# Performance work log

Measured on AMD Instinct MI355X. Metric: run time of the kernel, lower is better.

## Reference

```python
import jax, jax.numpy as jnp
import numpy as np

D_IN = 2048
D_SAE = 16384
N_RANGES = 4
CTX = 128  # batch == context_length
CHUNK = D_SAE // N_RANGES
LN_EPS = 1e-5


def setup_inputs() -> dict:
    key = jax.random.key(0)
    k1, k2, k3, k4 = jax.random.split(key, 4)
    acts = jax.random.normal(k1, (CTX, D_IN), dtype=jnp.float32)
    # orthogonal-init stand-ins: unit-variance columns
    W_enc_ranges = jax.random.normal(k2, (N_RANGES, D_IN, CHUNK), dtype=jnp.float32) / np.sqrt(D_IN)
    W_dec = jax.random.normal(k3, (D_SAE, D_IN), dtype=jnp.float32) / np.sqrt(D_SAE)
    pos_embeddings = jax.random.normal(k4, (N_RANGES, D_IN), dtype=jnp.float32) * 0.02
    return {
        "acts": acts,
        "W_enc_ranges": W_enc_ranges,
        "b_enc": jnp.zeros((D_SAE,), jnp.float32),
        "b_dec": jnp.zeros((D_IN,), jnp.float32),
        "pos_embeddings": pos_embeddings,
        "ln_weight": jnp.ones((D_SAE,), jnp.float32),
        "ln_bias": jnp.zeros((D_SAE,), jnp.float32),
        "W_dec": W_dec,
    }


def reference(acts, W_enc_ranges, b_enc, b_dec, pos_embeddings, ln_weight, ln_bias, W_dec):
    B, d_in = acts.shape
    n_ranges, _, chunk = W_enc_ranges.shape
    range_size = B // n_ranges  # positions are contiguous blocks per range
    d_sae = n_ranges * chunk

    # gather per position range: [n_ranges, range_size, d_in]
    x = acts.reshape(n_ranges, range_size, d_in)
    x = x + pos_embeddings[:, None, :] - b_dec  # (input + pos_emb) - b_dec

    # per-range GEMM + bias
    pre = jnp.einsum("rbd,rds->rbs", x, W_enc_ranges) + b_enc.reshape(n_ranges, 1, chunk)

    # per-range LayerNorm over the chunk (sliced gamma/beta), biased variance
    mu = jnp.mean(pre, axis=-1, keepdims=True)
    var = jnp.mean(jnp.square(pre - mu), axis=-1, keepdims=True)
    normed = (pre - mu) * jax.lax.rsqrt(var + LN_EPS)
    normed = normed * ln_weight.reshape(n_ranges, 1, chunk) + ln_bias.reshape(n_ranges, 1, chunk)
    feat = jax.nn.relu(normed)  # [n_ranges, range_size, chunk]

    # scatter into block-diagonal encoded [B, d_sae]
    encoded = jnp.zeros((B, d_sae), acts.dtype)
    for r in range(n_ranges):
        encoded = encoded.at[r * range_size:(r + 1) * range_size,
                             r * chunk:(r + 1) * chunk].set(feat[r])

    # decode
    decoded = encoded @ W_dec + b_dec
    return decoded
```

## Files before the change

### kernel.cpp

```cpp
#include <hip/hip_runtime.h>
#include <hip/hip_bf16.h>
#include <stdint.h>


#define D_IN   2048
#define CHUNK  4096
#define RS     32
#define LN_EPS 1e-5f

typedef __attribute__((ext_vector_type(8))) short bf16x8;
typedef __attribute__((ext_vector_type(4))) float f32x4;

#define AS1 __attribute__((address_space(1)))
#define AS3 __attribute__((address_space(3)))

__device__ __forceinline__ void gload_lds16(const float* g, float* l) {
  __builtin_amdgcn_global_load_lds((const AS1 unsigned int*)g,
                                   (AS3 unsigned int*)l, 16, 0, 0);
}

__device__ __forceinline__ unsigned short f2bf(float f) {
  unsigned int u = __float_as_uint(f);
  u += 0x7fffu + ((u >> 16) & 1u);
  return (unsigned short)(u >> 16);
}

__global__ __launch_bounds__(256) void prep_kernel(
    const float* __restrict__ acts, const float* __restrict__ pos,
    const float* __restrict__ bdec, unsigned short* __restrict__ xfrag) {
  unsigned tid = blockIdx.x * 256u + threadIdx.x;
  unsigned lane = tid & 63u, kt = (tid >> 6) & 63u, mt = (tid >> 12) & 1u, r = tid >> 13;
  unsigned m  = mt * 16 + (lane & 15u);
  unsigned k0 = kt * 32 + (lane >> 4) * 8;
  const float* ap = acts + (size_t)(r * RS + m) * D_IN + k0;
  const float* pp = pos  + (size_t)r * D_IN + k0;
  const float* bp = bdec + k0;
  bf16x8 v;
#pragma unroll
  for (int j = 0; j < 8; ++j) v[j] = (short)f2bf(ap[j] + pp[j] - bp[j]);
  *reinterpret_cast<bf16x8*>(xfrag + (size_t)tid * 8) = v;
}

__global__ __launch_bounds__(256) void enc_kernel(
    const unsigned short* __restrict__ xfrag, const float* __restrict__ Wenc,
    float* __restrict__ pre_part) {
  const unsigned r = blockIdx.x >> 8, h = (blockIdx.x >> 7) & 1u, nt = blockIdx.x & 127u;
  const unsigned n0 = nt * 32;
  const unsigned w = threadIdx.x >> 6, lane = threadIdx.x & 63u;
  const unsigned mt = w >> 1, nsub = w & 1u;
  const unsigned col = lane & 15u, g = lane >> 4;

  __shared__ float tiles[2][64 * 32];

  const unsigned srow = lane >> 3;
  const unsigned scol = (lane & 7u) * 4u;
  const float* gbase = Wenc + ((size_t)(r * D_IN + h * 1024)) * CHUNK + n0 + scol;
  const unsigned short* xa = xfrag + ((size_t)(r * 2 + mt) * 64) * 512 + (size_t)lane * 8;

  f32x4 acc = {0.f, 0.f, 0.f, 0.f};

  auto stageW = [&](unsigned s, unsigned b) {
#pragma unroll
    for (int l = 0; l < 2; ++l) {
      const float* gp = gbase + (size_t)(s * 64 + w * 16 + l * 8 + srow) * CHUNK;
      gload_lds16(gp, &tiles[b][(w * 2 + l) * 256]);
    }
  };

  stageW(0, 0);
  __syncthreads();

  unsigned cur = 0;
  for (unsigned s = 0; s < 16; ++s) {
    if (s + 1 < 16) stageW(s + 1, cur ^ 1);
#pragma unroll
    for (int t = 0; t < 2; ++t) {
      unsigned kt = h * 32 + s * 2 + t;
      bf16x8 a = *(const bf16x8*)(xa + (size_t)kt * 512);
      const float* tb = &tiles[cur][(t * 32 + g * 8) * 32 + nsub * 16 + col];
      bf16x8 bfrag;
#pragma unroll
      for (int j = 0; j < 8; ++j) bfrag[j] = (short)f2bf(tb[j * 32]);
      acc = __builtin_amdgcn_mfma_f32_16x16x32_bf16(a, bfrag, acc, 0, 0, 0);
    }
    __syncthreads();
    cur ^= 1;
  }

  float* pp = pre_part + (size_t)h * 128 * CHUNK;
  const unsigned nc = n0 + nsub * 16 + col;
#pragma unroll
  for (int i = 0; i < 4; ++i) {
    unsigned row = r * RS + mt * 16 + g * 4 + i;
    pp[(size_t)row * CHUNK + nc] = acc[i];
  }
}

__global__ __launch_bounds__(256) void lnpack_kernel(
    const float* __restrict__ pre_part, const float* __restrict__ benc,
    const float* __restrict__ gamma, const float* __restrict__ beta,
    unsigned short* __restrict__ featfrag) {
  const unsigned row = blockIdx.x;
  const unsigned r = row >> 5, m = row & 31u;
  const unsigned t = threadIdx.x;
  const unsigned c0 = t * 16;

  const float* p0 = pre_part + (size_t)row * CHUNK + c0;
  const float* p1 = p0 + (size_t)128 * CHUNK;
  const float* bb = benc + (size_t)r * CHUNK + c0;

  float v[16];
  float s = 0.f, q = 0.f;
#pragma unroll
  for (int j = 0; j < 16; ++j) {
    v[j] = p0[j] + p1[j] + bb[j];
    s += v[j]; q += v[j] * v[j];
  }
#pragma unroll
  for (int off = 1; off < 64; off <<= 1) {
    s += __shfl_xor(s, off, 64);
    q += __shfl_xor(q, off, 64);
  }
  __shared__ float ls[4], lq[4];
  if ((t & 63u) == 0) { ls[t >> 6] = s; lq[t >> 6] = q; }
  __syncthreads();
  s = ls[0] + ls[1] + ls[2] + ls[3];
  q = lq[0] + lq[1] + lq[2] + lq[3];
  float mu  = s * (1.f / CHUNK);
  float var = q * (1.f / CHUNK) - mu * mu;
  float rsd = rsqrtf(var + LN_EPS);

  const float* gp = gamma + (size_t)r * CHUNK + c0;
  const float* bp = beta  + (size_t)r * CHUNK + c0;
  const unsigned mt = m >> 4;
#pragma unroll
  for (int half = 0; half < 2; ++half) {
    bf16x8 o;
#pragma unroll
    for (int j = 0; j < 8; ++j) {
      float x = (v[half * 8 + j] - mu) * rsd * gp[half * 8 + j] + bp[half * 8 + j];
      o[j] = (short)f2bf(fmaxf(x, 0.f));
    }
    unsigned k = c0 + half * 8;
    unsigned kt = k >> 5, grp = (k >> 3) & 3u, ln = (m & 15u) + 16u * grp;
    *(bf16x8*)(featfrag + (((size_t)(r * 2 + mt) * 128 + kt) * 64 + ln) * 8) = o;
  }
}

__global__ __launch_bounds__(256) void dec_kernel(
    const unsigned short* __restrict__ featfrag, const float* __restrict__ Wdec,
    float* __restrict__ part) {
  const unsigned r = blockIdx.x >> 8, h = (blockIdx.x >> 6) & 3u, nt = blockIdx.x & 63u;
  const unsigned n0 = nt * 32;
  const unsigned w = threadIdx.x >> 6, lane = threadIdx.x & 63u;
  const unsigned mt = w >> 1, nsub = w & 1u;
  const unsigned col = lane & 15u, g = lane >> 4;

  __shared__ float tiles[2][64 * 32];

  const unsigned srow = lane >> 3;
  const unsigned scol = (lane & 7u) * 4u;
  const float* gbase = Wdec + ((size_t)(r * CHUNK + h * 1024)) * D_IN + n0 + scol;
  const unsigned short* fa = featfrag + ((size_t)(r * 2 + mt) * 128) * 512 + (size_t)lane * 8;

  f32x4 acc = {0.f, 0.f, 0.f, 0.f};

  auto stageW = [&](unsigned s, unsigned b) {
#pragma unroll
    for (int l = 0; l < 2; ++l) {
      const float* gp = gbase + (size_t)(s * 64 + w * 16 + l * 8 + srow) * D_IN;
      gload_lds16(gp, &tiles[b][(w * 2 + l) * 256]);
    }
  };

  stageW(0, 0);
  __syncthreads();

  unsigned cur = 0;
  for (unsigned s = 0; s < 16; ++s) {
    if (s + 1 < 16) stageW(s + 1, cur ^ 1);
#pragma unroll
    for (int t = 0; t < 2; ++t) {
      unsigned kt = h * 32 + s * 2 + t;
      bf16x8 a = *(const bf16x8*)(fa + (size_t)kt * 512);
      const float* tb = &tiles[cur][(t * 32 + g * 8) * 32 + nsub * 16 + col];
      bf16x8 bfrag;
#pragma unroll
      for (int j = 0; j < 8; ++j) bfrag[j] = (short)f2bf(tb[j * 32]);
      acc = __builtin_amdgcn_mfma_f32_16x16x32_bf16(a, bfrag, acc, 0, 0, 0);
    }
    __syncthreads();
    cur ^= 1;
  }

  float* pp = part + (size_t)h * 128 * D_IN;
  const unsigned nc = n0 + nsub * 16 + col;
#pragma unroll
  for (int i = 0; i < 4; ++i) {
    unsigned row = r * RS + mt * 16 + g * 4 + i;
    pp[(size_t)row * D_IN + nc] = acc[i];
  }
}

__global__ __launch_bounds__(256) void finish_kernel(
    const float* __restrict__ part, const float* __restrict__ bdec,
    float* __restrict__ out) {
  unsigned i = blockIdx.x * 256u + threadIdx.x;
  const size_t stride = (size_t)128 * D_IN / 4;
  f32x4 a0 = ((const f32x4*)part)[i];
  f32x4 a1 = ((const f32x4*)part)[i + stride];
  f32x4 a2 = ((const f32x4*)part)[i + 2 * stride];
  f32x4 a3 = ((const f32x4*)part)[i + 3 * stride];
  f32x4 c  = ((const f32x4*)bdec)[i & 511u];
  f32x4 o;
#pragma unroll
  for (int j = 0; j < 4; ++j) o[j] = a0[j] + a1[j] + a2[j] + a3[j] + c[j];
  ((f32x4*)out)[i] = o;
}

extern "C" void kernel_launch(void* const* d_in, const int* in_sizes, int n_in,
                              void* d_out, int out_size, void* d_ws, size_t ws_size,
                              hipStream_t stream) {
  const float* acts = (const float*)d_in[0];
  const float* Wenc = (const float*)d_in[1];
  const float* benc = (const float*)d_in[2];
  const float* bdec = (const float*)d_in[3];
  const float* pos  = (const float*)d_in[4];
  const float* lnw  = (const float*)d_in[5];
  const float* lnb  = (const float*)d_in[6];
  const float* Wdec = (const float*)d_in[7];
  float* out = (float*)d_out;

  char* ws = (char*)d_ws;
  unsigned short* xfrag   = (unsigned short*)ws;
  float* pre_part         = (float*)(ws + 512 * 1024);
  unsigned short* featfrg = (unsigned short*)(ws + 512 * 1024 + 4 * 1024 * 1024);
  float* part             = (float*)(ws + 512 * 1024 + 5 * 1024 * 1024);

  prep_kernel  <<<128,  256, 0, stream>>>(acts, pos, bdec, xfrag);
  enc_kernel   <<<1024, 256, 0, stream>>>(xfrag, Wenc, pre_part);
  lnpack_kernel<<<128,  256, 0, stream>>>(pre_part, benc, lnw, lnb, featfrg);
  dec_kernel   <<<1024, 256, 0, stream>>>(featfrg, Wdec, part);
  finish_kernel<<<256,  256, 0, stream>>>(part, bdec, out);
}
```

Before: 71.49 us.

## Split K across waves with private LDS tiles and reduce partials at end

Each wave in the encoder and decoder GEMM blocks now owns a private double-buffered LDS tile and a separate K-slice. It computes all four 16x16 output subtiles, reusing each converted B fragment across both M tiles. Per-iteration __syncthreads are replaced by per-wave vmcnt waits, and a single LDS reduction across waves runs at the end. This is meant to halve redundant fp32->bf16 conversions of W and remove block-wide barriers from the main loop. The cost is more accumulator registers, a final reduction pass, and reliance on hand-written waitcnt counts being correct.

```diff
diff --git a/kernel.cpp b/kernel.cpp
--- a/kernel.cpp
+++ b/kernel.cpp
@@ -24,6 +24,8 @@
   u += 0x7fffu + ((u >> 16) & 1u);
   return (unsigned short)(u >> 16);
 }
+
+#define MFMA16 __builtin_amdgcn_mfma_f32_16x16x32_bf16
 
 __global__ __launch_bounds__(256) void prep_kernel(
     const float* __restrict__ acts, const float* __restrict__ pos,
@@ -47,52 +49,92 @@
   const unsigned r = blockIdx.x >> 8, h = (blockIdx.x >> 7) & 1u, nt = blockIdx.x & 127u;
   const unsigned n0 = nt * 32;
   const unsigned w = threadIdx.x >> 6, lane = threadIdx.x & 63u;
-  const unsigned mt = w >> 1, nsub = w & 1u;
   const unsigned col = lane & 15u, g = lane >> 4;
 
-  __shared__ float tiles[2][64 * 32];
-
-  const unsigned srow = lane >> 3;
-  const unsigned scol = (lane & 7u) * 4u;
-  const float* gbase = Wenc + ((size_t)(r * D_IN + h * 1024)) * CHUNK + n0 + scol;
-  const unsigned short* xa = xfrag + ((size_t)(r * 2 + mt) * 64) * 512 + (size_t)lane * 8;
-
-  f32x4 acc = {0.f, 0.f, 0.f, 0.f};
+  __shared__ float smem[8192];
+  float* mytile = smem + w * 2048;
+
+  const unsigned srow = lane >> 3, scol = (lane & 7u) * 4u;
+  const float* gbase = Wenc
+      + ((size_t)(r * D_IN + h * 1024 + w * 32 + srow)) * CHUNK + n0 + scol;
+  const unsigned short* xa0 = xfrag + ((size_t)(r * 2 + 0) * 64) * 512 + (size_t)lane * 8;
+  const unsigned short* xa1 = xfrag + ((size_t)(r * 2 + 1) * 64) * 512 + (size_t)lane * 8;
+
+  f32x4 acc00 = {0.f,0.f,0.f,0.f}, acc01 = acc00, acc10 = acc00, acc11 = acc00;
 
   auto stageW = [&](unsigned s, unsigned b) {
 #pragma unroll
-    for (int l = 0; l < 2; ++l) {
-      const float* gp = gbase + (size_t)(s * 64 + w * 16 + l * 8 + srow) * CHUNK;
-      gload_lds16(gp, &tiles[b][(w * 2 + l) * 256]);
+    for (int l = 0; l < 4; ++l) {
+      const float* gp = gbase + (size_t)(s * 128 + l * 8) * CHUNK;
+      gload_lds16(gp, mytile + b * 1024 + l * 256);
     }
   };
 
+  bf16x8 aC0, aC1, aN0, aN1;
+  {
+    unsigned kt = h * 32 + w;
+    aC0 = *(const bf16x8*)(xa0 + (size_t)kt * 512);
+    aC1 = *(const bf16x8*)(xa1 + (size_t)kt * 512);
+  }
   stageW(0, 0);
-  __syncthreads();
-
-  unsigned cur = 0;
-  for (unsigned s = 0; s < 16; ++s) {
-    if (s + 1 < 16) stageW(s + 1, cur ^ 1);
-#pragma unroll
-    for (int t = 0; t < 2; ++t) {
-      unsigned kt = h * 32 + s * 2 + t;
-      bf16x8 a = *(const bf16x8*)(xa + (size_t)kt * 512);
-      const float* tb = &tiles[cur][(t * 32 + g * 8) * 32 + nsub * 16 + col];
-      bf16x8 bfrag;
-#pragma unroll
-      for (int j = 0; j < 8; ++j) bfrag[j] = (short)f2bf(tb[j * 32]);
-      acc = __builtin_amdgcn_mfma_f32_16x16x32_bf16(a, bfrag, acc, 0, 0, 0);
-    }
-    __syncthreads();
-    cur ^= 1;
-  }
-
-  float* pp = pre_part + (size_t)h * 128 * CHUNK;
-  const unsigned nc = n0 + nsub * 16 + col;
-#pragma unroll
-  for (int i = 0; i < 4; ++i) {
-    unsigned row = r * RS + mt * 16 + g * 4 + i;
-    pp[(size_t)row * CHUNK + nc] = acc[i];
+
+  unsigned buf = 0;
+#pragma unroll
+  for (int s = 0; s < 8; ++s) {
+    if (s < 7) {
+      unsigned kt = h * 32 + (s + 1) * 4 + w;
+      aN0 = *(const bf16x8*)(xa0 + (size_t)kt * 512);
+      aN1 = *(const bf16x8*)(xa1 + (size_t)kt * 512);
+      stageW(s + 1, buf ^ 1);
+      asm volatile("s_waitcnt vmcnt(6)" ::: "memory");
+    } else {
+      asm volatile("s_waitcnt vmcnt(0)" ::: "memory");
+    }
+    const float* tb = mytile + buf * 1024 + g * 8 * 32 + col;
+    bf16x8 b0, b1;
+#pragma unroll
+    for (int j = 0; j < 8; ++j) {
+      b0[j] = (short)f2bf(tb[j * 32]);
+      b1[j] = (short)f2bf(tb[j * 32 + 16]);
+    }
+    acc00 = MFMA16(aC0, b0, acc00, 0, 0, 0);
+    acc01 = MFMA16(aC0, b1, acc01, 0, 0, 0);
+    acc10 = MFMA16(aC1, b0, acc10, 0, 0, 0);
+    acc11 = MFMA16(aC1, b1, acc11, 0, 0, 0);
+    aC0 = aN0; aC1 = aN1; buf ^= 1;
+  }
+
+  __syncthreads();
+  float* red = smem;
+  if (w > 0) {
+#pragma unroll
+    for (int i = 0; i < 4; ++i) {
+      red[(((w - 1) * 4 + 0) * 64 + lane) * 4 + i] = acc00[i];
+      red[(((w - 1) * 4 + 1) * 64 + lane) * 4 + i] = acc01[i];
+      red[(((w - 1) * 4 + 2) * 64 + lane) * 4 + i] = acc10[i];
+      red[(((w - 1) * 4 + 3) * 64 + lane) * 4 + i] = acc11[i];
+    }
+  }
+  __syncthreads();
+  if (w == 0) {
+    for (int q = 0; q < 3; ++q)
+#pragma unroll
+      for (int i = 0; i < 4; ++i) {
+        acc00[i] += red[((q * 4 + 0) * 64 + lane) * 4 + i];
+        acc01[i] += red[((q * 4 + 1) * 64 + lane) * 4 + i];
+        acc10[i] += red[((q * 4 + 2) * 64 + lane) * 4 + i];
+        acc11[i] += red[((q * 4 + 3) * 64 + lane) * 4 + i];
+      }
+    float* pp = pre_part + (size_t)h * 128 * CHUNK;
+#pragma unroll
+    for (int i = 0; i < 4; ++i) {
+      unsigned row0 = r * RS + g * 4 + i;
+      unsigned row1 = row0 + 16;
+      pp[(size_t)row0 * CHUNK + n0 + col]      = acc00[i];
+      pp[(size_t)row0 * CHUNK + n0 + 16 + col] = acc01[i];
+      pp[(size_t)row1 * CHUNK + n0 + col]      = acc10[i];
+      pp[(size_t)row1 * CHUNK + n0 + 16 + col] = acc11[i];
+    }
   }
 }
 
@@ -153,52 +195,92 @@
   const unsigned r = blockIdx.x >> 8, h = (blockIdx.x >> 6) & 3u, nt = blockIdx.x & 63u;
   const unsigned n0 = nt * 32;
   const unsigned w = threadIdx.x >> 6, lane = threadIdx.x & 63u;
-  const unsigned mt = w >> 1, nsub = w & 1u;
   const unsigned col = lane & 15u, g = lane >> 4;
 
-  __shared__ float tiles[2][64 * 32];
-
-  const unsigned srow = lane >> 3;
-  const unsigned scol = (lane & 7u) * 4u;
-  const float* gbase = Wdec + ((size_t)(r * CHUNK + h * 1024)) * D_IN + n0 + scol;
-  const unsigned short* fa = featfrag + ((size_t)(r * 2 + mt) * 128) * 512 + (size_t)lane * 8;
-
-  f32x4 acc = {0.f, 0.f, 0.f, 0.f};
+  __shared__ float smem[8192];
+  float* mytile = smem + w * 2048;
+
+  const unsigned srow = lane >> 3, scol = (lane & 7u) * 4u;
+  const float* gbase = Wdec
+      + ((size_t)(r * CHUNK + h * 1024 + w * 32 + srow)) * D_IN + n0 + scol;
+  const unsigned short* fa0 = featfrag + ((size_t)(r * 2 + 0) * 128) * 512 + (size_t)lane * 8;
+  const unsigned short* fa1 = featfrag + ((size_t)(r * 2 + 1) * 128) * 512 + (size_t)lane * 8;
+
+  f32x4 acc00 = {0.f,0.f,0.f,0.f}, acc01 = acc00, acc10 = acc00, acc11 = acc00;
 
   auto stageW = [&](unsigned s, unsigned b) {
 #pragma unroll
-    for (int l = 0; l < 2; ++l) {
-      const float* gp = gbase + (size_t)(s * 64 + w * 16 + l * 8 + srow) * D_IN;
-      gload_lds16(gp, &tiles[b][(w * 2 + l) * 256]);
+    for (int l = 0; l < 4; ++l) {
+      const float* gp = gbase + (size_t)(s * 128 + l * 8) * D_IN;
+      gload_lds16(gp, mytile + b * 1024 + l * 256);
     }
   };
 
+  bf16x8 aC0, aC1, aN0, aN1;
+  {
+    unsigned kt = h * 32 + w;
+    aC0 = *(const bf16x8*)(fa0 + (size_t)kt * 512);
+    aC1 = *(const bf16x8*)(fa1 + (size_t)kt * 512);
+  }
   stageW(0, 0);
-  __syncthreads();
-
-  unsigned cur = 0;
-  for (unsigned s = 0; s < 16; ++s) {
-    if (s + 1 < 16) stageW(s + 1, cur ^ 1);
-#pragma unroll
-    for (int t = 0; t < 2; ++t) {
-      unsigned kt = h * 32 + s * 2 + t;
-      bf16x8 a = *(const bf16x8*)(fa + (size_t)kt * 512);
-      const float* tb = &tiles[cur][(t * 32 + g * 8) * 32 + nsub * 16 + col];
-      bf16x8 bfrag;
-#pragma unroll
-      for (int j = 0; j < 8; ++j) bfrag[j] = (short)f2bf(tb[j * 32]);
-      acc = __builtin_amdgcn_mfma_f32_16x16x32_bf16(a, bfrag, acc, 0, 0, 0);
-    }
-    __syncthreads();
-    cur ^= 1;
-  }
-
-  float* pp = part + (size_t)h * 128 * D_IN;
-  const unsigned nc = n0 + nsub * 16 + col;
-#pragma unroll
-  for (int i = 0; i < 4; ++i) {
-    unsigned row = r * RS + mt * 16 + g * 4 + i;
-    pp[(size_t)row * D_IN + nc] = acc[i];
+
+  unsigned buf = 0;
+#pragma unroll
+  for (int s = 0; s < 8; ++s) {
+    if (s < 7) {
+      unsigned kt = h * 32 + (s + 1) * 4 + w;
+      aN0 = *(const bf16x8*)(fa0 + (size_t)kt * 512);
+      aN1 = *(const bf16x8*)(fa1 + (size_t)kt * 512);
+      stageW(s + 1, buf ^ 1);
+      asm volatile("s_waitcnt vmcnt(6)" ::: "memory");
+    } else {
+      asm volatile("s_waitcnt vmcnt(0)" ::: "memory");
+    }
+    const float* tb = mytile + buf * 1024 + g * 8 * 32 + col;
+    bf16x8 b0, b1;
+#pragma unroll
+    for (int j = 0; j < 8; ++j) {
+      b0[j] = (short)f2bf(tb[j * 32]);
+      b1[j] = (short)f2bf(tb[j * 32 + 16]);
+    }
+    acc00 = MFMA16(aC0, b0, acc00, 0, 0, 0);
+    acc01 = MFMA16(aC0, b1, acc01, 0, 0, 0);
+    acc10 = MFMA16(aC1, b0, acc10, 0, 0, 0);
+    acc11 = MFMA16(aC1, b1, acc11, 0, 0, 0);
+    aC0 = aN0; aC1 = aN1; buf ^= 1;
+  }
+
+  __syncthreads();
+  float* red = smem;
+  if (w > 0) {
+#pragma unroll
+    for (int i = 0; i < 4; ++i) {
+      red[(((w - 1) * 4 + 0) * 64 + lane) * 4 + i] = acc00[i];
+      red[(((w - 1) * 4 + 1) * 64 + lane) * 4 + i] = acc01[i];
+      red[(((w - 1) * 4 + 2) * 64 + lane) * 4 + i] = acc10[i];
+      red[(((w - 1) * 4 + 3) * 64 + lane) * 4 + i] = acc11[i];
+    }
+  }
+  __syncthreads();
+  if (w == 0) {
+    for (int q = 0; q < 3; ++q)
+#pragma unroll
+      for (int i = 0; i < 4; ++i) {
+        acc00[i] += red[((q * 4 + 0) * 64 + lane) * 4 + i];
+        acc01[i] += red[((q * 4 + 1) * 64 + lane) * 4 + i];
+        acc10[i] += red[((q * 4 + 2) * 64 + lane) * 4 + i];
+        acc11[i] += red[((q * 4 + 3) * 64 + lane) * 4 + i];
+      }
+    float* pp = part + (size_t)h * 128 * D_IN;
+#pragma unroll
+    for (int i = 0; i < 4; ++i) {
+      unsigned row0 = r * RS + g * 4 + i;
+      unsigned row1 = row0 + 16;
+      pp[(size_t)row0 * D_IN + n0 + col]      = acc00[i];
+      pp[(size_t)row0 * D_IN + n0 + 16 + col] = acc01[i];
+      pp[(size_t)row1 * D_IN + n0 + col]      = acc10[i];
+      pp[(size_t)row1 * D_IN + n0 + 16 + col] = acc11[i];
+    }
   }
 }
 
```

Result: faster. 66.67 us (-6.7%).
